# Optimization experiments

Hardware: AMD Instinct MI355X
Metric: run time of the kernel (lower is better)

Reference implementation:

```python
import jax, jax.numpy as jnp
import numpy as np

N_NODES = 100000
N_EDGES = 3200000
IN_DIM = 512
HIDDEN = 16
N_CLASSES = 7


def setup_inputs() -> dict:
    key = jax.random.key(0)
    k1, k2, k3, k4 = jax.random.split(key, 4)
    x = jax.random.normal(k1, (N_NODES, IN_DIM), dtype=jnp.float32)
    edge_index = jax.random.randint(k2, (2, N_EDGES), 0, N_NODES, dtype=jnp.int32)
    W1 = jax.random.normal(k3, (IN_DIM, HIDDEN), dtype=jnp.float32) / np.sqrt(IN_DIM)
    b1 = jnp.zeros((HIDDEN,), dtype=jnp.float32)
    W2 = jax.random.normal(k4, (HIDDEN, N_CLASSES), dtype=jnp.float32) / np.sqrt(HIDDEN)
    b2 = jnp.zeros((N_CLASSES,), dtype=jnp.float32)
    return {"x": x, "edge_index": edge_index, "W1": W1, "b1": b1, "W2": W2, "b2": b2}


def _gcn_norm(edge_index, num_nodes):
    # Add self loops and compute symmetric normalization D^{-1/2} A D^{-1/2}
    loop = jnp.arange(num_nodes, dtype=edge_index.dtype)
    src = jnp.concatenate([edge_index[0], loop])
    dst = jnp.concatenate([edge_index[1], loop])
    deg = jax.ops.segment_sum(jnp.ones_like(dst, dtype=jnp.float32), dst,
                              num_segments=num_nodes)
    dinv = jnp.where(deg > 0, jax.lax.rsqrt(deg), 0.0)
    norm = dinv[src] * dinv[dst]  # [E + N]
    return src, dst, norm


def _gcn_conv(x, W, b, src, dst, norm, num_nodes):
    h = x @ W                                   # [N, out] dense GEMM first (PyG order)
    msg = h[src] * norm[:, None]                # gather + per-edge scale
    agg = jax.ops.segment_sum(msg, dst, num_segments=num_nodes)  # scatter-add
    return agg + b


def reference(x, edge_index, W1, b1, W2, b2):
    n = x.shape[0]
    src, dst, norm = _gcn_norm(edge_index, n)
    h = _gcn_conv(x, W1, b1, src, dst, norm, n)
    h = jax.nn.relu(h)
    # dropout is identity in eval mode (deterministic reference)
    out = _gcn_conv(h, W2, b2, src, dst, norm, n)
    return jax.nn.log_softmax(out, axis=1)
```

## Files before the change

### kernel.cpp

```cpp
#include <hip/hip_runtime.h>

#define N_NODES 100000
#define N_EDGES 3200000
#define IN_DIM  512
#define HIDDEN  16
#define NCLS    7

#define BSH     9
#define BNODES  512
#define NB      ((N_NODES + BNODES - 1) / BNODES)

#define EPB1    8192
#define NBLK1   ((N_EDGES + EPB1 - 1) / EPB1)
#define EPB2    4096
#define NBLK2   ((N_EDGES + EPB2 - 1) / EPB2)

#define GEMM1_BLOCKS 512

__global__ void k_zero(int* __restrict__ bcnt, int* __restrict__ rowstart) {
    int i = threadIdx.x;
    bcnt[i] = 0;
    if (i == 0) rowstart[N_NODES] = N_EDGES;
}

__global__ __launch_bounds__(256) void k_bcount(const int* __restrict__ dst,
                                                int* __restrict__ bcnt) {
    __shared__ int hist[256];
    int tid = threadIdx.x;
    hist[tid] = 0;
    __syncthreads();
    int e0 = blockIdx.x * EPB1;
    int n  = min(EPB1, N_EDGES - e0);
    for (int k = tid; k < n; k += 256)
        atomicAdd(&hist[dst[e0 + k] >> BSH], 1);
    __syncthreads();
    int c = hist[tid];
    if (c) atomicAdd(&bcnt[tid], c);
}

__global__ __launch_bounds__(256) void k_bscan(const int* __restrict__ bcnt,
                                               int* __restrict__ bstart,
                                               int* __restrict__ bcur) {
    __shared__ int s[256];
    int tid = threadIdx.x;
    int c = bcnt[tid];
    s[tid] = c;
    __syncthreads();
    for (int off = 1; off < 256; off <<= 1) {
        int t = (tid >= off) ? s[tid - off] : 0;
        __syncthreads();
        s[tid] += t;
        __syncthreads();
    }
    if (tid == 0) bstart[0] = 0;
    bstart[tid + 1] = s[tid];
    bcur[tid]       = s[tid] - c;
}

__global__ __launch_bounds__(256) void k_bscatter(const int* __restrict__ src,
                                                  const int* __restrict__ dst,
                                                  int* __restrict__ bcur,
                                                  unsigned int* __restrict__ ebuf) {
    __shared__ unsigned int pk[EPB2];
    __shared__ unsigned short bb[EPB2];
    __shared__ int hist[256], base[256], lcur[256];
    int tid = threadIdx.x;
    hist[tid] = 0; lcur[tid] = 0;
    __syncthreads();
    int e0 = blockIdx.x * EPB2;
    int n  = min(EPB2, N_EDGES - e0);
    for (int k = tid; k < n; k += 256) {
        int d = dst[e0 + k];
        int b = d >> BSH;
        pk[k] = ((unsigned int)src[e0 + k] << BSH) | (unsigned int)(d & (BNODES - 1));
        bb[k] = (unsigned short)b;
        atomicAdd(&hist[b], 1);
    }
    __syncthreads();
    int h = hist[tid];
    base[tid] = h ? atomicAdd(&bcur[tid], h) : 0;
    __syncthreads();
    for (int k = tid; k < n; k += 256) {
        int b = bb[k];
        int pos = atomicAdd(&lcur[b], 1);
        ebuf[base[b] + pos] = pk[k];
    }
}

__global__ __launch_bounds__(512) void k_bsort(const int* __restrict__ bstart,
                                               const unsigned int* __restrict__ ebuf,
                                               int* __restrict__ rowstart,
                                               float* __restrict__ dinv,
                                               int* __restrict__ csr_src) {
    __shared__ int hist[512], cur[512];
    int tid = threadIdx.x;
    int b   = blockIdx.x;
    int e0 = bstart[b], e1 = bstart[b + 1];
    hist[tid] = 0;
    __syncthreads();
    for (int i = e0 + tid; i < e1; i += 512)
        atomicAdd(&hist[ebuf[i] & (BNODES - 1)], 1);
    __syncthreads();
    int deg = hist[tid];
    for (int off = 1; off < 512; off <<= 1) {
        int t = (tid >= off) ? hist[tid - off] : 0;
        __syncthreads();
        hist[tid] += t;
        __syncthreads();
    }
    int excl = hist[tid] - deg;
    int node = (b << BSH) + tid;
    if (node < N_NODES) {
        rowstart[node] = e0 + excl;
        dinv[node]     = rsqrtf((float)(deg + 1));
    }
    cur[tid] = excl;
    __syncthreads();
    for (int i = e0 + tid; i < e1; i += 512) {
        unsigned int p = ebuf[i];
        int pos = atomicAdd(&cur[p & (BNODES - 1)], 1);
        csr_src[e0 + pos] = (int)(p >> BSH);
    }
}

__global__ __launch_bounds__(256, 2) void k_gemm1(
    const float* __restrict__ x, const float* __restrict__ W1,
    const float* __restrict__ dinv, float* __restrict__ h1s) {
    const int tid = threadIdx.x;
    const int l   = tid & 63;
    const int wid = blockIdx.x * 4 + (tid >> 6);
    const int nw  = GEMM1_BLOCKS * 4;

    float w[8][16];
#pragma unroll
    for (int q = 0; q < 4; ++q) {
#pragma unroll
        for (int c = 0; c < 4; ++c) {
            float4 t0 = *(const float4*)(W1 + (size_t)(4 * l + q) * 16 + 4 * c);
            w[q][4*c+0] = t0.x; w[q][4*c+1] = t0.y; w[q][4*c+2] = t0.z; w[q][4*c+3] = t0.w;
            float4 t1 = *(const float4*)(W1 + (size_t)(256 + 4 * l + q) * 16 + 4 * c);
            w[4+q][4*c+0] = t1.x; w[4+q][4*c+1] = t1.y; w[4+q][4*c+2] = t1.z; w[4+q][4*c+3] = t1.w;
        }
    }

    const int b0 = l & 1, b1 = (l >> 1) & 1, b2 = (l >> 2) & 1, b3 = (l >> 3) & 1;

    int n = wid;
    if (n >= N_NODES) return;
    const float* xr = x + (size_t)n * IN_DIM;
    float4 v0 = *(const float4*)(xr + 4 * l);
    float4 v1 = *(const float4*)(xr + 256 + 4 * l);

    for (;;) {
        int n2 = n + nw;
        int np = (n2 < N_NODES) ? n2 : n;
        const float* xp = x + (size_t)np * IN_DIM;
        float4 u0 = *(const float4*)(xp + 4 * l);
        float4 u1 = *(const float4*)(xp + 256 + 4 * l);

        float p[16];
#pragma unroll
        for (int j = 0; j < 16; ++j) {
            float a = v0.x * w[0][j];
            a = fmaf(v0.y, w[1][j], a);
            a = fmaf(v0.z, w[2][j], a);
            a = fmaf(v0.w, w[3][j], a);
            a = fmaf(v1.x, w[4][j], a);
            a = fmaf(v1.y, w[5][j], a);
            a = fmaf(v1.z, w[6][j], a);
            a = fmaf(v1.w, w[7][j], a);
            p[j] = a;
        }

        float q8[8];
#pragma unroll
        for (int m = 0; m < 8; ++m) {
            float keep = b0 ? p[2*m+1] : p[2*m];
            float give = b0 ? p[2*m]   : p[2*m+1];
            q8[m] = keep + __shfl_xor(give, 1);
        }
        float r4[4];
#pragma unroll
        for (int t = 0; t < 4; ++t) {
            float keep = b1 ? q8[2*t+1] : q8[2*t];
            float give = b1 ? q8[2*t]   : q8[2*t+1];
            r4[t] = keep + __shfl_xor(give, 2);
        }
        float s2[2];
#pragma unroll
        for (int u = 0; u < 2; ++u) {
            float keep = b2 ? r4[2*u+1] : r4[2*u];
            float give = b2 ? r4[2*u]   : r4[2*u+1];
            s2[u] = keep + __shfl_xor(give, 4);
        }
        float t0 = (b3 ? s2[1] : s2[0]) + __shfl_xor(b3 ? s2[0] : s2[1], 8);
        t0 += __shfl_xor(t0, 16);
        t0 += __shfl_xor(t0, 32);

        float di = dinv[n];
        if (l < 16) h1s[(size_t)n * 16 + l] = t0 * di;

        n = n2;
        if (n >= N_NODES) break;
        v0 = u0; v1 = u1;
    }
}

__global__ __launch_bounds__(256) void k_agg1(
    const int* __restrict__ rowstart, const int* __restrict__ csr_src,
    const float* __restrict__ h1s, const float* __restrict__ dinv,
    const float* __restrict__ b1, float* __restrict__ z) {
    int gid = blockIdx.x * 256 + threadIdx.x;
    int g = gid >> 4, j = gid & 15;
    bool valid = g < N_NODES;
    int n = valid ? g : (N_NODES - 1);
    int start = rowstart[n], end = rowstart[n + 1];
    float acc = h1s[(size_t)n * 16 + j];
    int i = start;
    for (; i + 8 <= end; i += 8) {
        int s[8];
#pragma unroll
        for (int u = 0; u < 8; ++u) s[u] = csr_src[i + u];
        float v[8];
#pragma unroll
        for (int u = 0; u < 8; ++u) v[u] = h1s[(size_t)s[u] * 16 + j];
        acc += ((v[0] + v[1]) + (v[2] + v[3])) + ((v[4] + v[5]) + (v[6] + v[7]));
    }
    for (; i < end; ++i)
        acc += h1s[(size_t)csr_src[i] * 16 + j];
    if (valid) {
        float v = dinv[n] * acc + b1[j];
        z[(size_t)n * 16 + j] = fmaxf(v, 0.f);
    }
}

__global__ __launch_bounds__(256) void k_layer2(
    const float* __restrict__ z, const float* __restrict__ W2,
    const float* __restrict__ dinv, float* __restrict__ h2s) {
    int n = blockIdx.x * 256 + threadIdx.x;
    if (n >= N_NODES) return;
    float zv[16];
#pragma unroll
    for (int k = 0; k < 16; k += 4) {
        float4 v = *(const float4*)(z + (size_t)n * 16 + k);
        zv[k] = v.x; zv[k+1] = v.y; zv[k+2] = v.z; zv[k+3] = v.w;
    }
    float di = dinv[n];
    float o[8];
#pragma unroll
    for (int jj = 0; jj < 7; ++jj) {
        float a = 0.f;
#pragma unroll
        for (int k = 0; k < 16; ++k) a = fmaf(zv[k], W2[k * 7 + jj], a);
        o[jj] = a * di;
    }
    o[7] = 0.f;
    *(float4*)(h2s + (size_t)n * 8 + 0) = make_float4(o[0], o[1], o[2], o[3]);
    *(float4*)(h2s + (size_t)n * 8 + 4) = make_float4(o[4], o[5], o[6], o[7]);
}

__global__ __launch_bounds__(256) void k_agg2(
    const int* __restrict__ rowstart, const int* __restrict__ csr_src,
    const float* __restrict__ h2s, const float* __restrict__ dinv,
    const float* __restrict__ b2, float* __restrict__ out) {
    int gid = blockIdx.x * 256 + threadIdx.x;
    int g = gid >> 3, j = gid & 7;
    bool valid = g < N_NODES;
    int n = valid ? g : (N_NODES - 1);
    int start = rowstart[n], end = rowstart[n + 1];
    float acc = h2s[(size_t)n * 8 + j];
    int i = start;
    for (; i + 8 <= end; i += 8) {
        int s[8];
#pragma unroll
        for (int u = 0; u < 8; ++u) s[u] = csr_src[i + u];
        float v[8];
#pragma unroll
        for (int u = 0; u < 8; ++u) v[u] = h2s[(size_t)s[u] * 8 + j];
        acc += ((v[0] + v[1]) + (v[2] + v[3])) + ((v[4] + v[5]) + (v[6] + v[7]));
    }
    for (; i < end; ++i)
        acc += h2s[(size_t)csr_src[i] * 8 + j];
    float v = dinv[n] * acc + ((j < 7) ? b2[j] : -1e30f);
    float m = v;
    m = fmaxf(m, __shfl_xor(m, 1));
    m = fmaxf(m, __shfl_xor(m, 2));
    m = fmaxf(m, __shfl_xor(m, 4));
    float e = (j < 7) ? expf(v - m) : 0.f;
    float ssum = e;
    ssum += __shfl_xor(ssum, 1);
    ssum += __shfl_xor(ssum, 2);
    ssum += __shfl_xor(ssum, 4);
    float ls = logf(ssum) + m;
    if (valid && j < 7) out[(size_t)n * 7 + j] = v - ls;
}

extern "C" void kernel_launch(void* const* d_in, const int* in_sizes, int n_in,
                              void* d_out, int out_size, void* d_ws, size_t ws_size,
                              hipStream_t stream) {
    const float* x  = (const float*)d_in[0];
    const int*   ei = (const int*)d_in[1];
    const float* W1 = (const float*)d_in[2];
    const float* b1 = (const float*)d_in[3];
    const float* W2 = (const float*)d_in[4];
    const float* b2 = (const float*)d_in[5];
    float* out = (float*)d_out;

    const int* src = ei;
    const int* dst = ei + N_EDGES;

    char* ws = (char*)d_ws;
    size_t o = 0;
    auto alloc = [&](size_t bytes) -> void* {
        void* p = ws + o;
        o = (o + bytes + 255) & ~(size_t)255;
        return p;
    };
    int*   bcnt     = (int*)alloc(256 * 4);
    int*   bstart   = (int*)alloc(257 * 4);
    int*   bcur     = (int*)alloc(256 * 4);
    int*   rowstart = (int*)alloc(((size_t)N_NODES + 1) * 4);
    float* dinv     = (float*)alloc((size_t)N_NODES * 4);
    int*   csr_src  = (int*)alloc((size_t)N_EDGES * 4);
    char*  uni      = (char*)alloc((size_t)N_EDGES * 4);
    unsigned int* ebuf = (unsigned int*)uni;
    float* h1s      = (float*)uni;
    float* z        = h1s + (size_t)N_NODES * 16;
    float* h2s      = (float*)alloc((size_t)N_NODES * 8 * 4);

    const int nb_n = (N_NODES + 255) / 256;

    k_zero    <<<1, 256, 0, stream>>>(bcnt, rowstart);
    k_bcount  <<<NBLK1, 256, 0, stream>>>(dst, bcnt);
    k_bscan   <<<1, 256, 0, stream>>>(bcnt, bstart, bcur);
    k_bscatter<<<NBLK2, 256, 0, stream>>>(src, dst, bcur, ebuf);
    k_bsort   <<<NB, 512, 0, stream>>>(bstart, ebuf, rowstart, dinv, csr_src);
    k_gemm1   <<<GEMM1_BLOCKS, 256, 0, stream>>>(x, W1, dinv, h1s);
    k_agg1    <<<(N_NODES * 16 + 255) / 256, 256, 0, stream>>>(rowstart, csr_src, h1s, dinv, b1, z);
    k_layer2  <<<nb_n, 256, 0, stream>>>(z, W2, dinv, h2s);
    k_agg2    <<<(N_NODES * 8 + 255) / 256, 256, 0, stream>>>(rowstart, csr_src, h2s, dinv, b2, out);
}
```

Baseline: 462.3 us.

## Fuse layer-2 transform into aggregation and deepen GEMM1 row prefetch

```diff
diff --git a/kernel.cpp b/kernel.cpp
--- a/kernel.cpp
+++ b/kernel.cpp
@@ -151,12 +151,23 @@
     float4 v0 = *(const float4*)(xr + 4 * l);
     float4 v1 = *(const float4*)(xr + 256 + 4 * l);
 
+    int n1 = n + nw;
+    float4 u0, u1;
+    {
+        int np = (n1 < N_NODES) ? n1 : n;
+        const float* xp = x + (size_t)np * IN_DIM;
+        u0 = *(const float4*)(xp + 4 * l);
+        u1 = *(const float4*)(xp + 256 + 4 * l);
+    }
+
     for (;;) {
-        int n2 = n + nw;
+        int n2 = n1 + nw;
         int np = (n2 < N_NODES) ? n2 : n;
         const float* xp = x + (size_t)np * IN_DIM;
-        float4 u0 = *(const float4*)(xp + 4 * l);
-        float4 u1 = *(const float4*)(xp + 256 + 4 * l);
+        float4 pf0 = *(const float4*)(xp + 4 * l);
+        float4 pf1 = *(const float4*)(xp + 256 + 4 * l);
+
+        float di = dinv[n];
 
         float p[16];
 #pragma unroll
@@ -197,23 +208,29 @@
         t0 += __shfl_xor(t0, 16);
         t0 += __shfl_xor(t0, 32);
 
-        float di = dinv[n];
         if (l < 16) h1s[(size_t)n * 16 + l] = t0 * di;
 
-        n = n2;
-        if (n >= N_NODES) break;
+        if (n1 >= N_NODES) break;
+        n = n1; n1 = n2;
         v0 = u0; v1 = u1;
+        u0 = pf0; u1 = pf1;
     }
 }
 
 __global__ __launch_bounds__(256) void k_agg1(
     const int* __restrict__ rowstart, const int* __restrict__ csr_src,
     const float* __restrict__ h1s, const float* __restrict__ dinv,
-    const float* __restrict__ b1, float* __restrict__ z) {
+    const float* __restrict__ b1, const float* __restrict__ W2,
+    float* __restrict__ h2s) {
     int gid = blockIdx.x * 256 + threadIdx.x;
     int g = gid >> 4, j = gid & 15;
     bool valid = g < N_NODES;
     int n = valid ? g : (N_NODES - 1);
+
+    float w2k[16];
+#pragma unroll
+    for (int k = 0; k < 16; ++k) w2k[k] = (j < 7) ? W2[k * 7 + j] : 0.f;
+
     int start = rowstart[n], end = rowstart[n + 1];
     float acc = h1s[(size_t)n * 16 + j];
     int i = start;
@@ -228,35 +245,17 @@
     }
     for (; i < end; ++i)
         acc += h1s[(size_t)csr_src[i] * 16 + j];
-    if (valid) {
-        float v = dinv[n] * acc + b1[j];
-        z[(size_t)n * 16 + j] = fmaxf(v, 0.f);
-    }
-}
-
-__global__ __launch_bounds__(256) void k_layer2(
-    const float* __restrict__ z, const float* __restrict__ W2,
-    const float* __restrict__ dinv, float* __restrict__ h2s) {
-    int n = blockIdx.x * 256 + threadIdx.x;
-    if (n >= N_NODES) return;
-    float zv[16];
-#pragma unroll
-    for (int k = 0; k < 16; k += 4) {
-        float4 v = *(const float4*)(z + (size_t)n * 16 + k);
-        zv[k] = v.x; zv[k+1] = v.y; zv[k+2] = v.z; zv[k+3] = v.w;
-    }
+
     float di = dinv[n];
-    float o[8];
-#pragma unroll
-    for (int jj = 0; jj < 7; ++jj) {
-        float a = 0.f;
-#pragma unroll
-        for (int k = 0; k < 16; ++k) a = fmaf(zv[k], W2[k * 7 + jj], a);
-        o[jj] = a * di;
-    }
-    o[7] = 0.f;
-    *(float4*)(h2s + (size_t)n * 8 + 0) = make_float4(o[0], o[1], o[2], o[3]);
-    *(float4*)(h2s + (size_t)n * 8 + 4) = make_float4(o[4], o[5], o[6], o[7]);
+    float zj = fmaxf(di * acc + b1[j], 0.f);
+
+    float o = 0.f;
+#pragma unroll
+    for (int k = 0; k < 16; ++k) {
+        float zk = __shfl(zj, k, 16);
+        o = fmaf(zk, w2k[k], o);
+    }
+    if (valid && j < 8) h2s[(size_t)n * 8 + j] = (j < 7) ? o * di : 0.f;
 }
 
 __global__ __launch_bounds__(256) void k_agg2(
@@ -325,10 +324,7 @@
     char*  uni      = (char*)alloc((size_t)N_EDGES * 4);
     unsigned int* ebuf = (unsigned int*)uni;
     float* h1s      = (float*)uni;
-    float* z        = h1s + (size_t)N_NODES * 16;
     float* h2s      = (float*)alloc((size_t)N_NODES * 8 * 4);
-
-    const int nb_n = (N_NODES + 255) / 256;
 
     k_zero    <<<1, 256, 0, stream>>>(bcnt, rowstart);
     k_bcount  <<<NBLK1, 256, 0, stream>>>(dst, bcnt);
@@ -336,7 +332,6 @@
     k_bscatter<<<NBLK2, 256, 0, stream>>>(src, dst, bcur, ebuf);
     k_bsort   <<<NB, 512, 0, stream>>>(bstart, ebuf, rowstart, dinv, csr_src);
     k_gemm1   <<<GEMM1_BLOCKS, 256, 0, stream>>>(x, W1, dinv, h1s);
-    k_agg1    <<<(N_NODES * 16 + 255) / 256, 256, 0, stream>>>(rowstart, csr_src, h1s, dinv, b1, z);
-    k_layer2  <<<nb_n, 256, 0, stream>>>(z, W2, dinv, h2s);
+    k_agg1    <<<(N_NODES * 16 + 255) / 256, 256, 0, stream>>>(rowstart, csr_src, h1s, dinv, b1, W2, h2s);
     k_agg2    <<<(N_NODES * 8 + 255) / 256, 256, 0, stream>>>(rowstart, csr_src, h2s, dinv, b2, out);
 }
```

New measurement: 456.6 us. About the same (-1.2%).
